# Kernel optimization log

Hardware: AMD Instinct MI355X
Metric: run time of the kernel (lower is better)

The kernel has to match this reference:

```python
import jax, jax.numpy as jnp
import numpy as np

N_HEAD = 16


def setup_inputs() -> dict:
    key = jax.random.key(0)
    k0, k1, k2, k3 = jax.random.split(key, 4)
    B, T, C = 2, 2048, 1024
    scale = 0.02
    x = jax.random.normal(k0, (B, T, C), dtype=jnp.float32)
    W_attn = jax.random.normal(k1, (C, 3 * C), dtype=jnp.float32) * scale
    b_attn = jnp.zeros((3 * C,), dtype=jnp.float32)
    W_proj = jax.random.normal(k2, (C, C), dtype=jnp.float32) * scale
    b_proj = jnp.zeros((C,), dtype=jnp.float32)
    return {"x": x, "W_attn": W_attn, "b_attn": b_attn, "W_proj": W_proj, "b_proj": b_proj}


def reference(x, W_attn, b_attn, W_proj, b_proj):
    B, T, C = x.shape
    H = N_HEAD
    hd = C // H
    # fused qkv projection
    qkv = x @ W_attn + b_attn                      # [B, T, 3C]
    q, k, v = jnp.split(qkv, 3, axis=-1)
    q = q.reshape(B, T, H, hd).transpose(0, 2, 1, 3)  # [B, H, T, hd]
    k = k.reshape(B, T, H, hd).transpose(0, 2, 1, 3)
    v = v.reshape(B, T, H, hd).transpose(0, 2, 1, 3)
    # scaled dot-product attention with causal mask (past_kv=None -> seq_len == T)
    att = jnp.einsum('bhqd,bhkd->bhqk', q, k) / jnp.sqrt(jnp.float32(hd))
    causal = jnp.tril(jnp.ones((T, T), dtype=bool))  # [T, T]
    att = jnp.where(causal[None, None, :, :], att, jnp.float32(-jnp.inf))
    att = jax.nn.softmax(att, axis=-1)
    y = jnp.einsum('bhqk,bhkd->bhqd', att, v)        # [B, H, T, hd]
    y = y.transpose(0, 2, 1, 3).reshape(B, T, C)
    y = y @ W_proj + b_proj
    return (y, k, v)  # (output, present_k, present_v)
```

## Files before the change

### kernel.cpp

```cpp
#include <hip/hip_runtime.h>
#include <hip/hip_bf16.h>

typedef __bf16 bf16;
typedef __bf16 bf16x8 __attribute__((ext_vector_type(8)));
typedef float f32x4 __attribute__((ext_vector_type(4)));

#define MFMA_BF16(a, b, c) __builtin_amdgcn_mfma_f32_16x16x32_bf16((a), (b), (c), 0, 0, 0)

#define SEQ_T 2048
#define DIM_C 1024

__global__ __launch_bounds__(256) void prep_kernel(
    const float* __restrict__ x, const float* __restrict__ Wa,
    const float* __restrict__ Wp, bf16* __restrict__ xbf,
    bf16* __restrict__ wat, bf16* __restrict__ wpt) {
  const int tid = threadIdx.x;
  const int bid = blockIdx.x;
  if (bid < 2048) {
    const size_t i = ((size_t)bid * 256 + tid) * 8;
    const f32x4 a = *(const f32x4*)(x + i);
    const f32x4 b = *(const f32x4*)(x + i + 4);
    bf16x8 r;
    r[0] = (bf16)a[0]; r[1] = (bf16)a[1]; r[2] = (bf16)a[2]; r[3] = (bf16)a[3];
    r[4] = (bf16)b[0]; r[5] = (bf16)b[1]; r[6] = (bf16)b[2]; r[7] = (bf16)b[3];
    *(bf16x8*)(xbf + i) = r;
  } else if (bid < 3584) {
    const int cid = (bid - 2048) * 256 + tid;
    const int kg = cid / 3072, n = cid - kg * 3072;
    bf16x8 r;
#pragma unroll
    for (int j = 0; j < 8; j++) r[j] = (bf16)Wa[(size_t)(kg * 8 + j) * 3072 + n];
    *(bf16x8*)(wat + (size_t)cid * 8) = r;
  } else {
    const int cid = (bid - 3584) * 256 + tid;
    const int kg = cid >> 10, n = cid & 1023;
    bf16x8 r;
#pragma unroll
    for (int j = 0; j < 8; j++) r[j] = (bf16)Wp[(size_t)(kg * 8 + j) * 1024 + n];
    *(bf16x8*)(wpt + (size_t)cid * 8) = r;
  }
}

template <int MODE, int BM>
__global__ __launch_bounds__(256) void gemm_kernel(
    const bf16* __restrict__ A, const bf16* __restrict__ Wt,
    const float* __restrict__ bias, float* __restrict__ out0,
    float* __restrict__ out1, bf16* __restrict__ bq, bf16* __restrict__ bk2,
    int M, int N, int K) {
  constexpr int MI = BM / 32;
  __shared__ bf16 As[BM][40];
  __shared__ bf16 Bt[128][40];

  const int tid = threadIdx.x;
  const int wid = tid >> 6, lane = tid & 63;
  const int quad = lane >> 4, l16 = lane & 15;
  const int wm = (wid >> 1) * (BM / 2), wn = (wid & 1) * 64;
  const int m0 = blockIdx.y * BM, n0 = blockIdx.x * 128;

  const f32x4 zero = {0.f, 0.f, 0.f, 0.f};
  f32x4 acc[MI][4];
#pragma unroll
  for (int i = 0; i < MI; i++)
#pragma unroll
    for (int j = 0; j < 4; j++) acc[i][j] = zero;

  for (int kk = 0; kk < K; kk += 32) {
    bf16x8 av[BM / 64], wv[2];
#pragma unroll
    for (int p = 0; p < BM / 64; p++) {
      const int s = tid + 256 * p;
      const int ar = s >> 2, aks = s & 3;
      av[p] = *(const bf16x8*)(A + (size_t)(m0 + ar) * K + kk + aks * 8);
    }
#pragma unroll
    for (int p = 0; p < 2; p++) {
      const int s = tid + 256 * p;
      const int bn = s & 127, bks = s >> 7;
      wv[p] = *(const bf16x8*)(Wt + ((size_t)((kk >> 3) + bks) * N + n0 + bn) * 8);
    }
    __syncthreads();
#pragma unroll
    for (int p = 0; p < BM / 64; p++) {
      const int s = tid + 256 * p;
      const int ar = s >> 2, aks = s & 3;
      *(bf16x8*)&As[ar][aks * 8] = av[p];
    }
#pragma unroll
    for (int p = 0; p < 2; p++) {
      const int s = tid + 256 * p;
      const int bn = s & 127, bks = s >> 7;
      *(bf16x8*)&Bt[bn][bks * 8] = wv[p];
    }
    __syncthreads();
    bf16x8 af[MI], bfr[4];
#pragma unroll
    for (int i = 0; i < MI; i++)
      af[i] = *(const bf16x8*)&As[wm + i * 16 + l16][quad * 8];
#pragma unroll
    for (int j = 0; j < 4; j++)
      bfr[j] = *(const bf16x8*)&Bt[wn + j * 16 + l16][quad * 8];
#pragma unroll
    for (int i = 0; i < MI; i++)
#pragma unroll
      for (int j = 0; j < 4; j++)
        acc[i][j] = MFMA_BF16(af[i], bfr[j], acc[i][j]);
  }

#pragma unroll
  for (int i = 0; i < MI; i++) {
#pragma unroll
    for (int j = 0; j < 4; j++) {
      const int col = n0 + wn + j * 16 + l16;
      const float bv = bias[col];
#pragma unroll
      for (int r = 0; r < 4; r++) {
        const int gm = m0 + wm + i * 16 + quad * 4 + r;
        const float v = acc[i][j][r] + bv;
        if (MODE == 0) {
          out0[(size_t)gm * N + col] = v;
        } else {
          const int which = col >> 10, c = col & 1023;
          const int h = c >> 6, d = c & 63;
          const int b = gm >> 11, t = gm & (SEQ_T - 1);
          const size_t idx = ((size_t)(b * 16 + h) * SEQ_T + t) * 64 + d;
          if (which == 0) {
            bq[idx] = (bf16)v;
          } else if (which == 1) {
            out0[idx] = v;
            bk2[idx] = (bf16)v;
          } else {
            out1[idx] = v;
          }
        }
      }
    }
  }
}

__global__ __launch_bounds__(512) void attn_kernel(
    const bf16* __restrict__ Qbf, const bf16* __restrict__ Kbf,
    const float* __restrict__ V, bf16* __restrict__ Y) {
  __shared__ bf16 Ks[2][64 * 72];
  __shared__ bf16 Vt[2][64 * 72];
  __shared__ bf16 Ps[8 * 16 * 72];

  const int tid = threadIdx.x;
  const int wid = tid >> 6, lane = tid & 63;
  const int quad = lane >> 4, l16 = lane & 15;

  const int qt = (blockIdx.y < 16) ? ((int)gridDim.x - 1 - (int)blockIdx.x)
                                   : (int)blockIdx.x;
  const int bh = blockIdx.y;
  const int q0 = qt * 128;
  const int b = bh >> 4, h = bh & 15;

  const bf16* qp = Qbf + (size_t)bh * SEQ_T * 64;
  const bf16* kp = Kbf + (size_t)bh * SEQ_T * 64;
  const float* vp = V + (size_t)bh * SEQ_T * 64;

  bf16x8 aq[2];
#pragma unroll
  for (int ks = 0; ks < 2; ks++)
    aq[ks] = *(const bf16x8*)(qp + (size_t)(q0 + wid * 16 + l16) * 64 + ks * 32 + quad * 8);

  bf16x8 bones;
#pragma unroll
  for (int j = 0; j < 8; j++) bones[j] = (bf16)1.0f;

  const f32x4 zero = {0.f, 0.f, 0.f, 0.f};
  f32x4 oacc[4], lacc;
  lacc = zero;
#pragma unroll
  for (int t = 0; t < 4; t++) oacc[t] = zero;

  const int last = 2 * qt + 1;
  bf16x8 kreg;
  f32x4 vf[2];

  auto load_tile = [&](int t) {
    const size_t base = (size_t)t * 64 * 64;
    kreg = *(const bf16x8*)(kp + base + (size_t)tid * 8);
    vf[0] = *(const f32x4*)(vp + base + (size_t)tid * 8);
    vf[1] = *(const f32x4*)(vp + base + (size_t)tid * 8 + 4);
  };
  auto stage_tile = [&](int buf) {
    const int key = tid >> 3, hs = tid & 7;
    *(bf16x8*)&Ks[buf][key * 72 + hs * 8] = kreg;
#pragma unroll
    for (int e = 0; e < 8; e++) {
      const float v = (e < 4) ? vf[0][e] : vf[1][e - 4];
      const int hr = hs * 8 + e;
      Vt[buf][hr * 72 + (((key >> 3) ^ hs) * 8) + (key & 7)] = (bf16)v;
    }
  };

  load_tile(0);
  stage_tile(0);
  load_tile(1);

  for (int it = 0; it <= last; ++it) {
    const int cur = it & 1;
    __syncthreads();
    if (it < last) stage_tile(cur ^ 1);
    if (it + 1 < last) load_tile(it + 2);

    const bool skip = (it == last) && (wid < 4);
    const bool dm = (it == 2 * qt && wid < 4) || (it == last && wid >= 4);

    f32x4 sa[4];
    if (!skip) {
#pragma unroll
      for (int nt = 0; nt < 4; nt++) {
        const bf16x8 bk0 = *(const bf16x8*)&Ks[cur][(nt * 16 + l16) * 72 + quad * 8];
        const bf16x8 bk1 = *(const bf16x8*)&Ks[cur][(nt * 16 + l16) * 72 + 32 + quad * 8];
        f32x4 s = MFMA_BF16(aq[0], bk0, zero);
        s = MFMA_BF16(aq[1], bk1, s);
        sa[nt] = s * 0.125f;
      }
      if (dm) {
#pragma unroll
        for (int nt = 0; nt < 4; nt++) {
          const int col = it * 64 + nt * 16 + l16;
#pragma unroll
          for (int r = 0; r < 4; r++) {
            const int row = q0 + wid * 16 + quad * 4 + r;
            if (col > row) sa[nt][r] = -1e30f;
          }
        }
      }
      bf16* pwb = &Ps[wid * 16 * 72];
#pragma unroll
      for (int nt = 0; nt < 4; nt++) {
        const int cb = nt * 16 + l16;
#pragma unroll
        for (int r = 0; r < 4; r++) {
          const int pr = quad * 4 + r;
          pwb[pr * 72 + (((cb >> 3) ^ (pr & 7)) * 8) + (cb & 7)] = (bf16)__expf(sa[nt][r]);
        }
      }
      bf16x8 ap[2];
#pragma unroll
      for (int ks = 0; ks < 2; ks++)
        ap[ks] = *(const bf16x8*)&pwb[l16 * 72 + (((ks * 4 + quad) ^ (l16 & 7)) * 8)];
      lacc = MFMA_BF16(ap[0], bones, lacc);
      lacc = MFMA_BF16(ap[1], bones, lacc);
#pragma unroll
      for (int nt = 0; nt < 4; nt++) {
        const int n = nt * 16 + l16;
#pragma unroll
        for (int ks = 0; ks < 2; ks++) {
          const bf16x8 bv = *(const bf16x8*)&Vt[cur][n * 72 + (((ks * 4 + quad) ^ (n >> 3)) * 8)];
          oacc[nt] = MFMA_BF16(ap[ks], bv, oacc[nt]);
        }
      }
    }
  }

  float inv[4];
#pragma unroll
  for (int r = 0; r < 4; r++) inv[r] = 1.f / lacc[r];
#pragma unroll
  for (int nt = 0; nt < 4; nt++) {
#pragma unroll
    for (int r = 0; r < 4; r++) {
      const int row = q0 + wid * 16 + quad * 4 + r;
      const int col = h * 64 + nt * 16 + l16;
      Y[((size_t)(b * SEQ_T + row)) * DIM_C + col] = (bf16)(oacc[nt][r] * inv[r]);
    }
  }
}

extern "C" void kernel_launch(void* const* d_in, const int* in_sizes, int n_in,
                              void* d_out, int out_size, void* d_ws, size_t ws_size,
                              hipStream_t stream) {
  (void)in_sizes; (void)n_in; (void)out_size; (void)ws_size;
  const float* x = (const float*)d_in[0];
  const float* W_attn = (const float*)d_in[1];
  const float* b_attn = (const float*)d_in[2];
  const float* W_proj = (const float*)d_in[3];
  const float* b_proj = (const float*)d_in[4];

  float* out = (float*)d_out;
  float* y_out = out;
  float* k_out = out + (size_t)4194304;
  float* v_out = out + (size_t)8388608;
  bf16* qbf = (bf16*)d_out;
  bf16* kbf = (bf16*)d_out + 4194304;
  bf16* y_att = (bf16*)d_in[0];
  bf16* xbf = (bf16*)d_ws;
  bf16* wat = xbf + 4194304;
  bf16* wpt = wat + 3145728;

  prep_kernel<<<4096, 256, 0, stream>>>(x, W_attn, W_proj, xbf, wat, wpt);
  gemm_kernel<1, 128><<<dim3(3072 / 128, 4096 / 128), 256, 0, stream>>>(
      xbf, wat, b_attn, k_out, v_out, qbf, kbf, 4096, 3072, 1024);
  attn_kernel<<<dim3(SEQ_T / 128, 32), 512, 0, stream>>>(qbf, kbf, v_out, y_att);
  gemm_kernel<0, 64><<<dim3(1024 / 128, 4096 / 64), 256, 0, stream>>>(
      y_att, wpt, b_proj, y_out, nullptr, nullptr, nullptr, 4096, 1024, 1024);
}
```

Measured before the change: 193.8 us.

## Use direct global-to-LDS loads in GEMM, bf16 V copy, exp2 softmax scaling

```diff
diff --git a/kernel.cpp b/kernel.cpp
--- a/kernel.cpp
+++ b/kernel.cpp
@@ -4,11 +4,17 @@
 typedef __bf16 bf16;
 typedef __bf16 bf16x8 __attribute__((ext_vector_type(8)));
 typedef float f32x4 __attribute__((ext_vector_type(4)));
+typedef unsigned int u32;
 
 #define MFMA_BF16(a, b, c) __builtin_amdgcn_mfma_f32_16x16x32_bf16((a), (b), (c), 0, 0, 0)
 
 #define SEQ_T 2048
 #define DIM_C 1024
+
+__device__ inline void gload16(const void* g, void* l) {
+  __builtin_amdgcn_global_load_lds((const __attribute__((address_space(1))) u32*)g,
+                                   (__attribute__((address_space(3))) u32*)l, 16, 0, 0);
+}
 
 __global__ __launch_bounds__(256) void prep_kernel(
     const float* __restrict__ x, const float* __restrict__ Wa,
@@ -46,16 +52,18 @@
     const bf16* __restrict__ A, const bf16* __restrict__ Wt,
     const float* __restrict__ bias, float* __restrict__ out0,
     float* __restrict__ out1, bf16* __restrict__ bq, bf16* __restrict__ bk2,
-    int M, int N, int K) {
+    bf16* __restrict__ bv2, int M, int N, int K) {
   constexpr int MI = BM / 32;
-  __shared__ bf16 As[BM][40];
-  __shared__ bf16 Bt[128][40];
+  constexpr int CA = BM / 64;
+  __shared__ bf16 As[BM][32];
+  __shared__ bf16 Bt[128][32];
 
   const int tid = threadIdx.x;
   const int wid = tid >> 6, lane = tid & 63;
   const int quad = lane >> 4, l16 = lane & 15;
   const int wm = (wid >> 1) * (BM / 2), wn = (wid & 1) * 64;
   const int m0 = blockIdx.y * BM, n0 = blockIdx.x * 128;
+  const int lr = lane >> 2, lks = lane & 3;
 
   const f32x4 zero = {0.f, 0.f, 0.f, 0.f};
   f32x4 acc[MI][4];
@@ -65,31 +73,18 @@
     for (int j = 0; j < 4; j++) acc[i][j] = zero;
 
   for (int kk = 0; kk < K; kk += 32) {
-    bf16x8 av[BM / 64], wv[2];
-#pragma unroll
-    for (int p = 0; p < BM / 64; p++) {
-      const int s = tid + 256 * p;
-      const int ar = s >> 2, aks = s & 3;
-      av[p] = *(const bf16x8*)(A + (size_t)(m0 + ar) * K + kk + aks * 8);
+    __syncthreads();
+#pragma unroll
+    for (int p = 0; p < CA; p++) {
+      const int c = wid * CA + p;
+      gload16(A + (size_t)(m0 + c * 16 + lr) * K + kk + lks * 8,
+              (bf16*)As + c * 512);
     }
 #pragma unroll
     for (int p = 0; p < 2; p++) {
-      const int s = tid + 256 * p;
-      const int bn = s & 127, bks = s >> 7;
-      wv[p] = *(const bf16x8*)(Wt + ((size_t)((kk >> 3) + bks) * N + n0 + bn) * 8);
-    }
-    __syncthreads();
-#pragma unroll
-    for (int p = 0; p < BM / 64; p++) {
-      const int s = tid + 256 * p;
-      const int ar = s >> 2, aks = s & 3;
-      *(bf16x8*)&As[ar][aks * 8] = av[p];
-    }
-#pragma unroll
-    for (int p = 0; p < 2; p++) {
-      const int s = tid + 256 * p;
-      const int bn = s & 127, bks = s >> 7;
-      *(bf16x8*)&Bt[bn][bks * 8] = wv[p];
+      const int c = wid * 2 + p;
+      gload16(Wt + ((size_t)((kk >> 3) + lks) * N + n0 + c * 16 + lr) * 8,
+              (bf16*)Bt + c * 512);
     }
     __syncthreads();
     bf16x8 af[MI], bfr[4];
@@ -124,12 +119,13 @@
           const int b = gm >> 11, t = gm & (SEQ_T - 1);
           const size_t idx = ((size_t)(b * 16 + h) * SEQ_T + t) * 64 + d;
           if (which == 0) {
-            bq[idx] = (bf16)v;
+            bq[idx] = (bf16)(v * 0.18033688f);
           } else if (which == 1) {
             out0[idx] = v;
             bk2[idx] = (bf16)v;
           } else {
             out1[idx] = v;
+            bv2[idx] = (bf16)v;
           }
         }
       }
@@ -139,7 +135,7 @@
 
 __global__ __launch_bounds__(512) void attn_kernel(
     const bf16* __restrict__ Qbf, const bf16* __restrict__ Kbf,
-    const float* __restrict__ V, bf16* __restrict__ Y) {
+    const bf16* __restrict__ V, bf16* __restrict__ Y) {
   __shared__ bf16 Ks[2][64 * 72];
   __shared__ bf16 Vt[2][64 * 72];
   __shared__ bf16 Ps[8 * 16 * 72];
@@ -156,7 +152,7 @@
 
   const bf16* qp = Qbf + (size_t)bh * SEQ_T * 64;
   const bf16* kp = Kbf + (size_t)bh * SEQ_T * 64;
-  const float* vp = V + (size_t)bh * SEQ_T * 64;
+  const bf16* vp = V + (size_t)bh * SEQ_T * 64;
 
   bf16x8 aq[2];
 #pragma unroll
@@ -174,23 +170,20 @@
   for (int t = 0; t < 4; t++) oacc[t] = zero;
 
   const int last = 2 * qt + 1;
-  bf16x8 kreg;
-  f32x4 vf[2];
+  bf16x8 kreg, vreg;
 
   auto load_tile = [&](int t) {
     const size_t base = (size_t)t * 64 * 64;
     kreg = *(const bf16x8*)(kp + base + (size_t)tid * 8);
-    vf[0] = *(const f32x4*)(vp + base + (size_t)tid * 8);
-    vf[1] = *(const f32x4*)(vp + base + (size_t)tid * 8 + 4);
+    vreg = *(const bf16x8*)(vp + base + (size_t)tid * 8);
   };
   auto stage_tile = [&](int buf) {
     const int key = tid >> 3, hs = tid & 7;
     *(bf16x8*)&Ks[buf][key * 72 + hs * 8] = kreg;
 #pragma unroll
     for (int e = 0; e < 8; e++) {
-      const float v = (e < 4) ? vf[0][e] : vf[1][e - 4];
       const int hr = hs * 8 + e;
-      Vt[buf][hr * 72 + (((key >> 3) ^ hs) * 8) + (key & 7)] = (bf16)v;
+      Vt[buf][hr * 72 + (((key >> 3) ^ hs) * 8) + (key & 7)] = vreg[e];
     }
   };
 
@@ -214,8 +207,7 @@
         const bf16x8 bk0 = *(const bf16x8*)&Ks[cur][(nt * 16 + l16) * 72 + quad * 8];
         const bf16x8 bk1 = *(const bf16x8*)&Ks[cur][(nt * 16 + l16) * 72 + 32 + quad * 8];
         f32x4 s = MFMA_BF16(aq[0], bk0, zero);
-        s = MFMA_BF16(aq[1], bk1, s);
-        sa[nt] = s * 0.125f;
+        sa[nt] = MFMA_BF16(aq[1], bk1, s);
       }
       if (dm) {
 #pragma unroll
@@ -235,7 +227,7 @@
 #pragma unroll
         for (int r = 0; r < 4; r++) {
           const int pr = quad * 4 + r;
-          pwb[pr * 72 + (((cb >> 3) ^ (pr & 7)) * 8) + (cb & 7)] = (bf16)__expf(sa[nt][r]);
+          pwb[pr * 72 + (((cb >> 3) ^ (pr & 7)) * 8) + (cb & 7)] = (bf16)exp2f(sa[nt][r]);
         }
       }
       bf16x8 ap[2];
@@ -287,14 +279,16 @@
   bf16* qbf = (bf16*)d_out;
   bf16* kbf = (bf16*)d_out + 4194304;
   bf16* y_att = (bf16*)d_in[0];
+  bf16* vbf = (bf16*)d_in[0] + 4194304;
   bf16* xbf = (bf16*)d_ws;
   bf16* wat = xbf + 4194304;
   bf16* wpt = wat + 3145728;
 
   prep_kernel<<<4096, 256, 0, stream>>>(x, W_attn, W_proj, xbf, wat, wpt);
   gemm_kernel<1, 128><<<dim3(3072 / 128, 4096 / 128), 256, 0, stream>>>(
-      xbf, wat, b_attn, k_out, v_out, qbf, kbf, 4096, 3072, 1024);
-  attn_kernel<<<dim3(SEQ_T / 128, 32), 512, 0, stream>>>(qbf, kbf, v_out, y_att);
+      xbf, wat, b_attn, k_out, v_out, qbf, kbf, vbf, 4096, 3072, 1024);
+  attn_kernel<<<dim3(SEQ_T / 128, 32), 512, 0, stream>>>(qbf, kbf, vbf, y_att);
   gemm_kernel<0, 64><<<dim3(1024 / 128, 4096 / 64), 256, 0, stream>>>(
-      y_att, wpt, b_proj, y_out, nullptr, nullptr, nullptr, 4096, 1024, 1024);
-}
+      y_att, wpt, b_proj, y_out, nullptr, nullptr, nullptr, nullptr,
+      4096, 1024, 1024);
+}
```

Result: slower. 208.4 us (+7.5%).
